# Kernel optimization log

Hardware: AMD Instinct MI355X
Metric: run time of the kernel (lower is better)

Reference implementation:

```python
import jax, jax.numpy as jnp
import numpy as np

DIM = 256
HEADS = 8
HEAD_DIM = DIM // HEADS
WS = 7            # window size
SHIFT = 3         # shift size
H = 56
W = 56
B = 32
WA = WS * WS      # window area = 49
NWH, NWW = H // WS, W // WS
NW = NWH * NWW    # windows per image


def _make_attn_mask():
    # replicate the torch mask construction for the shifted windows
    img = np.zeros((H, W), dtype=np.float32)
    cnt = 0
    for hs in (slice(0, -WS), slice(-WS, -SHIFT), slice(-SHIFT, None)):
        for ws_ in (slice(0, -WS), slice(-WS, -SHIFT), slice(-SHIFT, None)):
            img[hs, ws_] = cnt
            cnt += 1
    mw = img.reshape(NWH, WS, NWW, WS).transpose(0, 2, 1, 3).reshape(-1, WA)  # (nW, 49)
    diff = mw[:, None, :] - mw[:, :, None]                                    # (nW, 49, 49)
    return np.where(diff != 0, -100.0, 0.0).astype(np.float32)


def _make_rel_index():
    coords = np.stack(np.meshgrid(np.arange(WS), np.arange(WS), indexing='ij')).reshape(2, -1)
    rel = coords[:, :, None] - coords[:, None, :]        # (2, 49, 49)
    rel = rel.transpose(1, 2, 0) + (WS - 1)              # shift to >= 0
    rel[..., 0] *= 2 * WS - 1
    return rel.sum(-1).astype(np.int32)                  # (49, 49) in [0, 169)


def setup_inputs() -> dict:
    key = jax.random.key(0)
    ks = jax.random.split(key, 12)
    s = 0.02
    inp = {
        'x': jax.random.normal(ks[0], (B, H, W, DIM), dtype=jnp.float32),
        'ln1_w': jnp.ones((DIM,), jnp.float32), 'ln1_b': jnp.zeros((DIM,), jnp.float32),
        'qkv_w': s * jax.random.normal(ks[1], (3 * DIM, DIM), jnp.float32),
        'qkv_b': jnp.zeros((3 * DIM,), jnp.float32),
        'rpb_table': s * jax.random.normal(ks[2], ((2 * WS - 1) ** 2, HEADS), jnp.float32),
        'proj_w': s * jax.random.normal(ks[3], (DIM, DIM), jnp.float32),
        'proj_b': jnp.zeros((DIM,), jnp.float32),
        'ln2_w': jnp.ones((DIM,), jnp.float32), 'ln2_b': jnp.zeros((DIM,), jnp.float32),
        'fc1_w': s * jax.random.normal(ks[4], (4 * DIM, DIM), jnp.float32),
        'fc1_b': jnp.zeros((4 * DIM,), jnp.float32),
        'ln3_w': jnp.ones((4 * DIM,), jnp.float32), 'ln3_b': jnp.zeros((4 * DIM,), jnp.float32),
        'fc2_w': s * jax.random.normal(ks[5], (DIM, 4 * DIM), jnp.float32),
        'fc2_b': jnp.zeros((DIM,), jnp.float32),
        'attn_mask': jnp.asarray(_make_attn_mask()),     # (nW, 49, 49)
        'rel_index': jnp.asarray(_make_rel_index()),     # (49, 49) int32
    }
    return inp


def _ln(x, w, b, eps=1e-5):
    m = jnp.mean(x, axis=-1, keepdims=True)
    v = jnp.mean((x - m) ** 2, axis=-1, keepdims=True)
    return (x - m) * jax.lax.rsqrt(v + eps) * w + b


def reference(x, ln1_w, ln1_b, qkv_w, qkv_b, rpb_table, proj_w, proj_b,
              ln2_w, ln2_b, fc1_w, fc1_b, ln3_w, ln3_b, fc2_w, fc2_b,
              attn_mask, rel_index):
    Bn, Hn, Wn, C = x.shape
    # ---- attention branch ----
    y = _ln(x, ln1_w, ln1_b)
    sh = jnp.roll(y, (-SHIFT, -SHIFT), axis=(1, 2))
    # window partition: (B, H, W, C) -> (B*nW, 49, C)
    win = sh.reshape(Bn, NWH, WS, NWW, WS, C).transpose(0, 1, 3, 2, 4, 5).reshape(Bn * NW, WA, C)
    qkv = win @ qkv_w.T + qkv_b                              # (Bw, 49, 3C)
    qkv = qkv.reshape(Bn * NW, WA, 3, HEADS, HEAD_DIM).transpose(2, 0, 3, 1, 4)
    q, k, v = qkv[0], qkv[1], qkv[2]                         # (Bw, h, 49, d)
    scale = HEAD_DIM ** -0.5
    attn = jnp.einsum('bhqd,bhkd->bhqk', q * scale, k)       # (Bw, h, 49, 49)
    bias = rpb_table[rel_index]                              # (49, 49, h)
    attn = attn + jnp.transpose(bias, (2, 0, 1))[None]
    attn = attn.reshape(Bn, NW, HEADS, WA, WA) + attn_mask[None, :, None]
    attn = jax.nn.softmax(attn, axis=-1).reshape(Bn * NW, HEADS, WA, WA)
    out = jnp.einsum('bhqk,bhkd->bhqd', attn, v)             # (Bw, h, 49, d)
    out = out.transpose(0, 2, 1, 3).reshape(Bn * NW, WA, C)
    out = out @ proj_w.T + proj_b
    # window reverse + un-shift
    out = out.reshape(Bn, NWH, NWW, WS, WS, C).transpose(0, 1, 3, 2, 4, 5).reshape(Bn, Hn, Wn, C)
    out = jnp.roll(out, (SHIFT, SHIFT), axis=(1, 2))
    x = x + out
    # ---- MLP branch (note: extra LayerNorm inside MLP per source) ----
    z = _ln(x, ln2_w, ln2_b)
    h = jax.nn.gelu(z @ fc1_w.T + fc1_b, approximate=False)
    h = _ln(h, ln3_w, ln3_b)
    x = x + (h @ fc2_w.T + fc2_b)
    return x
```

## Files before the change

### kernel.cpp

```cpp
#include <hip/hip_runtime.h>
#include <hip/hip_bf16.h>
#include <math.h>

typedef __attribute__((ext_vector_type(8))) short bf16x8;
typedef __attribute__((ext_vector_type(4))) float f32x4;
typedef __attribute__((ext_vector_type(4))) float f4;
typedef __attribute__((ext_vector_type(8))) unsigned short us8;
typedef __attribute__((ext_vector_type(4))) unsigned short us4;
typedef unsigned short u16;
typedef unsigned int u32;

#define HEADS 8
#define SHIFT_ 3
#define HIMG 56
#define WIMG 56
#define WA 49
#define NTOK 100352
#define NPAIR 16384

static __device__ __forceinline__ float bf2f(u16 v){ return __uint_as_float(((u32)v)<<16); }
static __device__ __forceinline__ u16 f2bf(float f){
  u32 u = __float_as_uint(f);
  return (u16)((u + 0x7fffu + ((u>>16)&1u)) >> 16);
}
static __device__ __forceinline__ float wsum(float v){
  #pragma unroll
  for (int off=32; off>0; off>>=1) v += __shfl_xor(v, off, 64);
  return v;
}
static __device__ __forceinline__ void glds16(const u16* g, u16* l){
  __builtin_amdgcn_global_load_lds(
      (const __attribute__((address_space(1))) unsigned int*)g,
      (__attribute__((address_space(3))) unsigned int*)l, 16, 0, 0);
}
static __device__ __forceinline__ int tok2pix(int row){
  int bw = row / 49, t = row - bw*49;
  int b  = bw >> 6,  w = bw & 63;
  int wh = w >> 3,   ww = w & 7;
  int th = t / 7,    tw = t - th*7;
  int r = wh*7 + th + SHIFT_; if (r >= HIMG) r -= HIMG;
  int c = ww*7 + tw + SHIFT_; if (c >= WIMG) c -= WIMG;
  return (b*HIMG + r)*WIMG + c;
}

template<int C, int ISBF>
__global__ void ln_stats_kernel(const void* __restrict__ srcv, float* __restrict__ stats){
  int wave = threadIdx.x >> 6, lane = threadIdx.x & 63;
  int tok = blockIdx.x*4 + wave;
  float s=0.f, s2=0.f;
  if (ISBF == 0){
    const float* p = (const float*)srcv + (size_t)tok*C;
    #pragma unroll
    for (int i=0;i<C/256;i++){
      f4 v = *(const f4*)(p + lane*4*(C/256) + i*4);
      #pragma unroll
      for (int e=0;e<4;e++){ float f=v[e]; s+=f; s2+=f*f; }
    }
  } else {
    const u16* p = (const u16*)srcv + (size_t)tok*C;
    #pragma unroll
    for (int i=0;i<C/512;i++){
      us8 v = *(const us8*)(p + lane*8*(C/512) + i*8);
      #pragma unroll
      for (int e=0;e<8;e++){ float f=bf2f(v[e]); s+=f; s2+=f*f; }
    }
  }
  s = wsum(s); s2 = wsum(s2);
  if (lane==0){
    float mean = s/(float)C;
    float var  = s2/(float)C - mean*mean;
    stats[2*tok]   = mean;
    stats[2*tok+1] = rsqrtf(var + 1e-5f);
  }
}

__global__ void ln_apply_kernel(const float* __restrict__ src, u16* __restrict__ dst){
  int wave = threadIdx.x >> 6, lane = threadIdx.x & 63;
  int tok = blockIdx.x*4 + wave;
  const float* p = src + (size_t)tok*256;
  f4 a = *(const f4*)(p + lane*4);
  float s = a[0]+a[1]+a[2]+a[3];
  float s2 = a[0]*a[0]+a[1]*a[1]+a[2]*a[2]+a[3]*a[3];
  s = wsum(s); s2 = wsum(s2);
  float mean = s*(1.f/256.f);
  float var  = s2*(1.f/256.f) - mean*mean;
  float rstd = rsqrtf(var + 1e-5f);
  us4 o;
  #pragma unroll
  for (int e=0;e<4;e++) o[e] = f2bf((a[e]-mean)*rstd);
  *(us4*)(dst + (size_t)tok*256 + lane*4) = o;
}

__global__ void prep_weights(
    const float* __restrict__ qkv_w, const float* __restrict__ qkv_b,
    const float* __restrict__ ln1w,  const float* __restrict__ ln1b,
    const float* __restrict__ fc1_w, const float* __restrict__ fc1_b,
    const float* __restrict__ ln2w,  const float* __restrict__ ln2b,
    const float* __restrict__ fc2_w, const float* __restrict__ fc2_b,
    const float* __restrict__ ln3w,  const float* __restrict__ ln3b,
    const float* __restrict__ proj_w, const float* __restrict__ proj_b,
    u16* __restrict__ wq, float* __restrict__ bq,
    u16* __restrict__ w1, float* __restrict__ b1,
    u16* __restrict__ w2, float* __restrict__ b2,
    u16* __restrict__ wp, float* __restrict__ bp)
{
  int wave = threadIdx.x>>6, lane = threadIdx.x&63;
  int n = blockIdx.x*4 + wave;
  const float *W,*lw,*lb,*bs; u16* WO; float* BO; int K, row, noln;
  if (n < 768)      { W=qkv_w; lw=ln1w; lb=ln1b; bs=qkv_b; WO=wq; BO=bq; K=256;  row=n;      noln=0; }
  else if (n < 1792){ W=fc1_w; lw=ln2w; lb=ln2b; bs=fc1_b; WO=w1; BO=b1; K=256;  row=n-768;  noln=0; }
  else if (n < 2048){ W=fc2_w; lw=ln3w; lb=ln3b; bs=fc2_b; WO=w2; BO=b2; K=1024; row=n-1792; noln=0; }
  else              { W=proj_w; lw=nullptr; lb=nullptr; bs=proj_b; WO=wp; BO=bp; K=256; row=n-2048; noln=1; }
  float dot = 0.f;
  for (int k=lane; k<K; k+=64){
    float wv = W[(size_t)row*K + k];
    if (noln){
      WO[(size_t)row*K + k] = f2bf(wv);
    } else {
      dot += wv * lb[k];
      WO[(size_t)row*K + k] = f2bf(wv * lw[k]);
    }
  }
  dot = wsum(dot);
  if (lane==0) BO[row] = bs[row] + dot;
}

template<int SMODE, int EPI>
__global__ __launch_bounds__(256)
void gemm4(const void* __restrict__ Av, const u16* __restrict__ Bt,
           const float* __restrict__ stats, const float* __restrict__ biasf,
           const float* __restrict__ resid, void* __restrict__ outv,
           int K, int NT, int CHUNK)
{
  constexpr int BM=128, BN=128, BK=64;
  __shared__ u16 smem[32768];
  int b = blockIdx.x;
  int linear = (b & 7)*CHUNK + (b >> 3);
  int mt = linear / NT, nt = linear - mt*NT;
  int m0 = mt*BM, n0 = nt*BN;
  int tid  = threadIdx.x;
  int lane = tid & 63, wave = tid >> 6;
  int wr = wave >> 1, wc = wave & 1;
  int lc16 = lane & 15, g = lane >> 4;
  int nsteps = K >> 6;

  const u16* asrc[4];
  const u16* bsrc[4];
  #pragma unroll
  for (int i=0;i<4;i++){
    int c = tid + i*256;
    int row = c >> 3, ch = (c & 7) ^ (row & 7);
    if (SMODE <= 1){
      int grow = (SMODE==0) ? tok2pix(m0+row) : (m0+row);
      asrc[i] = (const u16*)Av + (size_t)grow*K + ch*8;
    }
    bsrc[i] = Bt + (size_t)(n0+row)*K + ch*8;
  }
  float smean[4], srstd[4];
  if (SMODE >= 2){
    #pragma unroll
    for (int i=0;i<4;i++){
      int grow = m0 + ((tid + i*256) >> 3);
      smean[i] = stats[2*grow]; srstd[i] = stats[2*grow+1];
    }
  }

  f32x4 acc[4][4];
  #pragma unroll
  for (int i=0;i<4;i++)
    #pragma unroll
    for (int j=0;j<4;j++){ acc[i][j][0]=0.f; acc[i][j][1]=0.f; acc[i][j][2]=0.f; acc[i][j][3]=0.f; }

  us8 rcur[4]; f4 rcurf[4][2];
  if (SMODE <= 1){
    #pragma unroll
    for (int i=0;i<4;i++) glds16(asrc[i], smem + i*2048 + wave*512);
  } else {
    #pragma unroll
    for (int i=0;i<4;i++){
      int c = tid + i*256; int row = c>>3, ch = c&7;
      if (SMODE==2) rcur[i] = *(const us8*)((const u16*)Av + (size_t)(m0+row)*K + ch*8);
      else {
        const float* ap = (const float*)Av + (size_t)(m0+row)*K + ch*8;
        rcurf[i][0] = *(const f4*)ap; rcurf[i][1] = *(const f4*)(ap+4);
      }
    }
  }
  #pragma unroll
  for (int i=0;i<4;i++) glds16(bsrc[i], smem + 16384 + i*2048 + wave*512);

  for (int t=0; t<nsteps; ++t){
    int cur = t & 1;
    int curoff = cur << 13;
    int nxtoff = (cur^1) << 13;
    us8 rnext[4]; f4 rnextf[4][2];
    int kt1 = (t+1) << 6;
    if (t+1 < nsteps){
      if (SMODE <= 1){
        #pragma unroll
        for (int i=0;i<4;i++) glds16(asrc[i]+kt1, smem + nxtoff + i*2048 + wave*512);
      } else {
        #pragma unroll
        for (int i=0;i<4;i++){
          int c = tid + i*256; int row = c>>3, ch = c&7;
          if (SMODE==2) rnext[i] = *(const us8*)((const u16*)Av + (size_t)(m0+row)*K + kt1 + ch*8);
          else {
            const float* ap = (const float*)Av + (size_t)(m0+row)*K + kt1 + ch*8;
            rnextf[i][0] = *(const f4*)ap; rnextf[i][1] = *(const f4*)(ap+4);
          }
        }
      }
      #pragma unroll
      for (int i=0;i<4;i++) glds16(bsrc[i]+kt1, smem + 16384 + nxtoff + i*2048 + wave*512);
    }
    if (SMODE >= 2){
      #pragma unroll
      for (int i=0;i<4;i++){
        int c = tid + i*256; int row = c>>3, ch = c&7;
        us8 o;
        #pragma unroll
        for (int e=0;e<8;e++){
          float fv = (SMODE==2) ? bf2f(rcur[i][e]) : rcurf[i][e>>2][e&3];
          o[e] = f2bf((fv - smean[i])*srstd[i]);
        }
        u32 byte = (u32)(row*128 + ch*16) ^ ((u32)(row&7)<<4);
        *(us8*)(smem + curoff + (byte>>1)) = o;
      }
      asm volatile("s_waitcnt lgkmcnt(0)" ::: "memory");
    }
    if (t+1 < nsteps) asm volatile("s_waitcnt vmcnt(8)" ::: "memory");
    else              asm volatile("s_waitcnt vmcnt(0)" ::: "memory");
    __builtin_amdgcn_s_barrier();
    asm volatile("" ::: "memory");
    __builtin_amdgcn_sched_barrier(0);
    const u16* Ap = smem + curoff;
    const u16* Bp = smem + 16384 + curoff;
    #pragma unroll
    for (int kk=0; kk<2; kk++){
      bf16x8 af[4], bfr[4];
      #pragma unroll
      for (int mi=0;mi<4;mi++){
        int r = wr*64 + mi*16 + lc16;
        u32 byte = (u32)(r*128 + kk*64 + g*16) ^ ((u32)(r&7)<<4);
        af[mi] = *(const bf16x8*)(Ap + (byte>>1));
      }
      #pragma unroll
      for (int ni=0;ni<4;ni++){
        int r = wc*64 + ni*16 + lc16;
        u32 byte = (u32)(r*128 + kk*64 + g*16) ^ ((u32)(r&7)<<4);
        bfr[ni] = *(const bf16x8*)(Bp + (byte>>1));
      }
      #pragma unroll
      for (int mi=0;mi<4;mi++)
        #pragma unroll
        for (int ni=0;ni<4;ni++)
          acc[mi][ni] = __builtin_amdgcn_mfma_f32_16x16x32_bf16(af[mi], bfr[ni], acc[mi][ni], 0, 0, 0);
    }
    asm volatile("" ::: "memory");
    __builtin_amdgcn_s_barrier();
    asm volatile("" ::: "memory");
    if (SMODE >= 2 && t+1 < nsteps){
      #pragma unroll
      for (int i=0;i<4;i++){
        if (SMODE==2) rcur[i] = rnext[i];
        else { rcurf[i][0] = rnextf[i][0]; rcurf[i][1] = rnextf[i][1]; }
      }
    }
  }

  int lr = lane >> 4;
  if (EPI==0 || EPI==2){
    u16* Cs = smem;
    #pragma unroll
    for (int mi=0;mi<4;mi++){
      #pragma unroll
      for (int ni=0;ni<4;ni++){
        int cl = wc*64 + ni*16 + lc16;
        float bv = biasf[n0 + cl];
        #pragma unroll
        for (int j=0;j<4;j++){
          int rl = wr*64 + mi*16 + lr*4 + j;
          float v = acc[mi][ni][j] + bv;
          if (EPI==2) v = 0.5f*v*(1.f + erff(v*0.70710678118654752f));
          u32 byte = (u32)(rl*256 + cl*2) ^ ((u32)(rl&7)<<4);
          Cs[byte>>1] = f2bf(v);
        }
      }
    }
    __syncthreads();
    #pragma unroll
    for (int i=0;i<8;i++){
      int c = tid + i*256;
      int rl = c>>4, c0 = (c&15)*8;
      u32 byte = (u32)(rl*256 + c0*2) ^ ((u32)(rl&7)<<4);
      us8 v = *(const us8*)(Cs + (byte>>1));
      int row = m0 + rl, col = n0 + c0;
      if (EPI==0){
        int which = col>>8, hh = (col>>5)&7, d0 = col&31;
        int bwi = row/49, t = row - bwi*49;
        *(us8*)((u16*)outv + ((size_t)which*NPAIR + bwi*8 + hh)*(WA*32) + t*32 + d0) = v;
      } else {
        *(us8*)((u16*)outv + (size_t)row*1024 + col) = v;
      }
    }
  } else {
    float* Cs = (float*)smem;
    #pragma unroll
    for (int mi=0;mi<4;mi++){
      #pragma unroll
      for (int ni=0;ni<4;ni++){
        int cl = wc*64 + ni*16 + lc16;
        float bv = biasf[n0 + cl];
        #pragma unroll
        for (int j=0;j<4;j++){
          int rl = wr*64 + mi*16 + lr*4 + j;
          u32 byte = (u32)(rl*512 + cl*4) ^ ((u32)(rl&7)<<4);
          *(float*)((char*)Cs + byte) = acc[mi][ni][j] + bv;
        }
      }
    }
    __syncthreads();
    #pragma unroll
    for (int p=0;p<16;p++){
      int c = tid + p*256;
      int row = c>>5, ch = c&31;
      u32 byte = (u32)(row*512 + ch*16) ^ ((u32)(row&7)<<4);
      f4 v = *(const f4*)((const char*)Cs + byte);
      int grow = m0 + row, col = n0 + ch*4;
      size_t addr;
      if (EPI==1) addr = (size_t)tok2pix(grow)*256 + col;
      else        addr = (size_t)grow*256 + col;
      f4 rr = *(const f4*)(resid + addr);
      v += rr;
      *(f4*)((float*)outv + addr) = v;
    }
  }
}

__global__ void attn_mfma_kernel(
    const u16* __restrict__ qkv,
    const float* __restrict__ rpb,
    const int* __restrict__ rel,
    const float* __restrict__ mask,
    u16* __restrict__ outb)
{
  __shared__ u16 Kls[4][64*32];
  __shared__ u16 Vt [4][32*64];
  __shared__ u16 Pls[4][64*64];
  int wave = threadIdx.x>>6, lane = threadIdx.x&63;
  int pair = blockIdx.x*4 + wave;
  int bw = pair>>3, h = pair&7, w = bw&63;
  int lc = lane&15, g = lane>>4;
  const u16* qg = qkv + (size_t)pair*(WA*32);
  const u16* kg = qg + (size_t)NPAIR*(WA*32);
  const u16* vg = qg + (size_t)2*NPAIR*(WA*32);
  u16* Kp = &Kls[wave][0];
  u16* Vp = &Vt[wave][0];
  u16* Pp = &Pls[wave][0];

  #pragma unroll
  for (int i=0;i<4;i++){
    int idx = i*64 + lane;
    int r = idx>>2, seg = idx&3;
    us8 kv, vv;
    if (r < WA){
      kv = *(const us8*)(kg + r*32 + seg*8);
      vv = *(const us8*)(vg + r*32 + seg*8);
    } else {
      #pragma unroll
      for (int e=0;e<8;e++){ kv[e]=0; vv[e]=0; }
    }
    *(us8*)(Kp + r*32 + seg*8) = kv;
    #pragma unroll
    for (int e=0;e<8;e++){
      int d = seg*8 + e;
      u32 byte = ((u32)(d*128 + r*2)) ^ ((u32)(d&7)<<4);
      Vp[byte>>1] = vv[e];
    }
  }

  bf16x8 qa[4];
  #pragma unroll
  for (int mi=0;mi<4;mi++){
    int r = mi*16 + lc;
    if (r < WA) qa[mi] = *(const bf16x8*)(qg + r*32 + g*8);
    else { bf16x8 z;
           #pragma unroll
           for (int e=0;e<8;e++) z[e]=0; qa[mi]=z; }
  }

  f32x4 acc[4][4];
  #pragma unroll
  for (int i=0;i<4;i++)
    #pragma unroll
    for (int j=0;j<4;j++){ acc[i][j][0]=0.f; acc[i][j][1]=0.f; acc[i][j][2]=0.f; acc[i][j][3]=0.f; }
  __syncthreads();
  #pragma unroll
  for (int ni=0;ni<4;ni++){
    bf16x8 kb = *(const bf16x8*)(Kp + (ni*16+lc)*32 + g*8);
    #pragma unroll
    for (int mi=0;mi<4;mi++)
      acc[mi][ni] = __builtin_amdgcn_mfma_f32_16x16x32_bf16(qa[mi], kb, acc[mi][ni], 0, 0, 0);
  }

  const float scale = 0.17677669529663689f;
  float rinv[4][4];
  #pragma unroll
  for (int mi=0;mi<4;mi++){
    #pragma unroll
    for (int jr=0;jr<4;jr++){
      int i = mi*16 + g*4 + jr;
      float sv[4];
      #pragma unroll
      for (int ni=0;ni<4;ni++){
        int j = ni*16 + lc;
        float s;
        if (i < WA && j < WA){
          s = acc[mi][ni][jr]*scale + rpb[rel[i*WA+j]*8 + h] + mask[((size_t)w*WA + i)*WA + j];
        } else s = -1e9f;
        sv[ni] = s;
      }
      float mx = fmaxf(fmaxf(sv[0],sv[1]), fmaxf(sv[2],sv[3]));
      #pragma unroll
      for (int off=1; off<16; off<<=1) mx = fmaxf(mx, __shfl_xor(mx, off, 64));
      float sum = 0.f;
      #pragma unroll
      for (int ni=0;ni<4;ni++){ sv[ni] = __expf(sv[ni]-mx); sum += sv[ni]; }
      #pragma unroll
      for (int off=1; off<16; off<<=1) sum += __shfl_xor(sum, off, 64);
      rinv[mi][jr] = 1.f/sum;
      #pragma unroll
      for (int ni=0;ni<4;ni++){
        int j = ni*16 + lc;
        u32 byte = ((u32)(i*128 + j*2)) ^ ((u32)(i&7)<<4);
        Pp[byte>>1] = f2bf(sv[ni]);
      }
    }
  }

  bf16x8 vb[2][2];
  #pragma unroll
  for (int kk=0;kk<2;kk++)
    #pragma unroll
    for (int ni=0;ni<2;ni++){
      int d = ni*16 + lc;
      u32 byte = ((u32)(d*128 + kk*64 + g*16)) ^ ((u32)(d&7)<<4);
      vb[kk][ni] = *(const bf16x8*)(Vp + (byte>>1));
    }
  f32x4 aco[4][2];
  #pragma unroll
  for (int i=0;i<4;i++)
    #pragma unroll
    for (int j=0;j<2;j++){ aco[i][j][0]=0.f; aco[i][j][1]=0.f; aco[i][j][2]=0.f; aco[i][j][3]=0.f; }
  #pragma unroll
  for (int mi=0;mi<4;mi++){
    int r = mi*16 + lc;
    #pragma unroll
    for (int kk=0;kk<2;kk++){
      u32 byte = ((u32)(r*128 + kk*64 + g*16)) ^ ((u32)(r&7)<<4);
      bf16x8 pa = *(const bf16x8*)(Pp + (byte>>1));
      #pragma unroll
      for (int ni=0;ni<2;ni++)
        aco[mi][ni] = __builtin_amdgcn_mfma_f32_16x16x32_bf16(pa, vb[kk][ni], aco[mi][ni], 0, 0, 0);
    }
  }

  u16* Op = Kp;
  #pragma unroll
  for (int mi=0;mi<4;mi++){
    #pragma unroll
    for (int jr=0;jr<4;jr++){
      int i = mi*16 + g*4 + jr;
      if (i < WA){
        float rv = rinv[mi][jr];
        #pragma unroll
        for (int ni=0;ni<2;ni++)
          Op[i*32 + ni*16 + lc] = f2bf(aco[mi][ni][jr]*rv);
      }
    }
  }
  __syncthreads();
  size_t obase = (size_t)(bw*WA)*256 + h*32;
  #pragma unroll
  for (int i=0;i<4;i++){
    int c = i*64 + lane;
    if (c < WA*4){
      int t = c>>2, seg = c&3;
      *(us8*)(outb + obase + (size_t)t*256 + seg*8) = *(const us8*)(Op + t*32 + seg*8);
    }
  }
}

extern "C" void kernel_launch(void* const* d_in, const int* in_sizes, int n_in,
                              void* d_out, int out_size, void* d_ws, size_t ws_size,
                              hipStream_t stream) {
  const float* x      = (const float*)d_in[0];
  const float* ln1w   = (const float*)d_in[1];
  const float* ln1b   = (const float*)d_in[2];
  const float* qkv_w  = (const float*)d_in[3];
  const float* qkv_b  = (const float*)d_in[4];
  const float* rpb    = (const float*)d_in[5];
  const float* proj_w = (const float*)d_in[6];
  const float* proj_b = (const float*)d_in[7];
  const float* ln2w   = (const float*)d_in[8];
  const float* ln2b   = (const float*)d_in[9];
  const float* fc1_w  = (const float*)d_in[10];
  const float* fc1_b  = (const float*)d_in[11];
  const float* ln3w   = (const float*)d_in[12];
  const float* ln3b   = (const float*)d_in[13];
  const float* fc2_w  = (const float*)d_in[14];
  const float* fc2_b  = (const float*)d_in[15];
  const float* amask  = (const float*)d_in[16];
  const int*   rel    = (const int*)d_in[17];
  float* out = (float*)d_out;

  char* ws = (char*)d_ws;
  float* statsC = (float*)(ws);
  float* statsB = (float*)(ws +  802816);
  float* bq     = (float*)(ws + 1605632);
  float* b1     = (float*)(ws + 1608704);
  float* b2     = (float*)(ws + 1612800);
  float* bp     = (float*)(ws + 1613824);
  u16*   wq     = (u16*)  (ws + 1614848);
  u16*   w1     = (u16*)  (ws + 2008064);
  u16*   w2     = (u16*)  (ws + 2532352);
  u16*   wp     = (u16*)  (ws + 3056640);
  const size_t P0 = 3187712;
  u16*   qkvbuf = (u16*)(ws + P0);
  u16*   attno  = (u16*)(ws + P0 + 154140672);
  u16*   xb     = (u16*)(ws + P0 + 154140672);
  u16*   hbuf   = (u16*)(ws + P0);
  u16*   x1b    = (u16*)(ws + P0 + 205520896);
  const int bigws = (ws_size >= (size_t)(P0 + 205520896ull + 51380224ull));

  prep_weights<<<576,256,0,stream>>>(qkv_w,qkv_b,ln1w,ln1b, fc1_w,fc1_b,ln2w,ln2b,
                                     fc2_w,fc2_b,ln3w,ln3b, proj_w,proj_b,
                                     wq,bq, w1,b1, w2,b2, wp,bp);
  ln_apply_kernel<<<NTOK/4,256,0,stream>>>(x, xb);
  gemm4<0,0><<<784*6,256,0,stream>>>(xb, wq, nullptr, bq, nullptr, qkvbuf, 256, 6, 588);
  attn_mfma_kernel<<<NPAIR/4,256,0,stream>>>(qkvbuf, rpb, rel, amask, attno);
  gemm4<1,1><<<784*2,256,0,stream>>>(attno, wp, nullptr, bp, x, out, 256, 2, 196);
  if (bigws){
    ln_apply_kernel<<<NTOK/4,256,0,stream>>>(out, x1b);
    gemm4<1,2><<<784*8,256,0,stream>>>(x1b, w1, nullptr, b1, nullptr, hbuf, 256, 8, 784);
  } else {
    ln_stats_kernel<256,0><<<NTOK/4,256,0,stream>>>(out, statsB);
    gemm4<3,2><<<784*8,256,0,stream>>>(out, w1, statsB, b1, nullptr, hbuf, 256, 8, 784);
  }
  ln_stats_kernel<1024,1><<<NTOK/4,256,0,stream>>>(hbuf, statsC);
  gemm4<2,3><<<784*2,256,0,stream>>>(hbuf, w2, statsC, b2, out, out, 1024, 2, 196);
}
```

Baseline: 625.8 us.

## Single-buffer GEMM LDS to raise occupancy, use polynomial GELU and fast reciprocal

Halves the GEMM shared memory by dropping LDS double buffering, switching to a load-sync-compute loop, and requests four blocks per CU through launch bounds. The fp32 epilogue is split into two 64-column halves so it fits the smaller LDS buffer. Exact erf GELU is replaced with an Abramowitz-Stegun polynomial approximation, and the softmax division uses the hardware reciprocal. The goal is more resident waves to hide latency, at the cost of losing the explicit prefetch overlap inside each block and a slight loss of accuracy.

```diff
diff --git a/kernel.cpp b/kernel.cpp
--- a/kernel.cpp
+++ b/kernel.cpp
@@ -41,6 +41,15 @@
   int r = wh*7 + th + SHIFT_; if (r >= HIMG) r -= HIMG;
   int c = ww*7 + tw + SHIFT_; if (c >= WIMG) c -= WIMG;
   return (b*HIMG + r)*WIMG + c;
+}
+static __device__ __forceinline__ float gelu_f(float x){
+  float z  = 0.70710678118654752f * x;
+  float az = fabsf(z);
+  float t  = __builtin_amdgcn_rcpf(1.0f + 0.3275911f*az);
+  float p  = t*(0.254829592f + t*(-0.284496736f + t*(1.421413741f + t*(-1.453152027f + t*1.061405429f))));
+  float er = 1.0f - p*__expf(-z*z);
+  er = (x < 0.0f) ? -er : er;
+  return 0.5f*x*(1.0f + er);
 }
 
 template<int C, int ISBF>
@@ -126,14 +135,16 @@
 }
 
 template<int SMODE, int EPI>
-__global__ __launch_bounds__(256)
-void gemm4(const void* __restrict__ Av, const u16* __restrict__ Bt,
+__global__ __launch_bounds__(256,4)
+void gemm5(const void* __restrict__ Av, const u16* __restrict__ Bt,
            const float* __restrict__ stats, const float* __restrict__ biasf,
            const float* __restrict__ resid, void* __restrict__ outv,
            int K, int NT, int CHUNK)
 {
   constexpr int BM=128, BN=128, BK=64;
-  __shared__ u16 smem[32768];
+  __shared__ u16 smem[16384];
+  u16* As = smem;
+  u16* Bs = smem + 8192;
   int b = blockIdx.x;
   int linear = (b & 7)*CHUNK + (b >> 3);
   int mt = linear / NT, nt = linear - mt*NT;
@@ -172,10 +183,7 @@
     for (int j=0;j<4;j++){ acc[i][j][0]=0.f; acc[i][j][1]=0.f; acc[i][j][2]=0.f; acc[i][j][3]=0.f; }
 
   us8 rcur[4]; f4 rcurf[4][2];
-  if (SMODE <= 1){
-    #pragma unroll
-    for (int i=0;i<4;i++) glds16(asrc[i], smem + i*2048 + wave*512);
-  } else {
+  if (SMODE >= 2){
     #pragma unroll
     for (int i=0;i<4;i++){
       int c = tid + i*256; int row = c>>3, ch = c&7;
@@ -186,34 +194,13 @@
       }
     }
   }
-  #pragma unroll
-  for (int i=0;i<4;i++) glds16(bsrc[i], smem + 16384 + i*2048 + wave*512);
 
   for (int t=0; t<nsteps; ++t){
-    int cur = t & 1;
-    int curoff = cur << 13;
-    int nxtoff = (cur^1) << 13;
-    us8 rnext[4]; f4 rnextf[4][2];
-    int kt1 = (t+1) << 6;
-    if (t+1 < nsteps){
-      if (SMODE <= 1){
-        #pragma unroll
-        for (int i=0;i<4;i++) glds16(asrc[i]+kt1, smem + nxtoff + i*2048 + wave*512);
-      } else {
-        #pragma unroll
-        for (int i=0;i<4;i++){
-          int c = tid + i*256; int row = c>>3, ch = c&7;
-          if (SMODE==2) rnext[i] = *(const us8*)((const u16*)Av + (size_t)(m0+row)*K + kt1 + ch*8);
-          else {
-            const float* ap = (const float*)Av + (size_t)(m0+row)*K + kt1 + ch*8;
-            rnextf[i][0] = *(const f4*)ap; rnextf[i][1] = *(const f4*)(ap+4);
-          }
-        }
-      }
-      #pragma unroll
-      for (int i=0;i<4;i++) glds16(bsrc[i]+kt1, smem + 16384 + nxtoff + i*2048 + wave*512);
-    }
-    if (SMODE >= 2){
+    int kt = t << 6;
+    if (SMODE <= 1){
+      #pragma unroll
+      for (int i=0;i<4;i++) glds16(asrc[i]+kt, As + i*2048 + wave*512);
+    } else {
       #pragma unroll
       for (int i=0;i<4;i++){
         int c = tid + i*256; int row = c>>3, ch = c&7;
@@ -224,48 +211,74 @@
           o[e] = f2bf((fv - smean[i])*srstd[i]);
         }
         u32 byte = (u32)(row*128 + ch*16) ^ ((u32)(row&7)<<4);
-        *(us8*)(smem + curoff + (byte>>1)) = o;
-      }
-      asm volatile("s_waitcnt lgkmcnt(0)" ::: "memory");
-    }
-    if (t+1 < nsteps) asm volatile("s_waitcnt vmcnt(8)" ::: "memory");
-    else              asm volatile("s_waitcnt vmcnt(0)" ::: "memory");
-    __builtin_amdgcn_s_barrier();
-    asm volatile("" ::: "memory");
-    __builtin_amdgcn_sched_barrier(0);
-    const u16* Ap = smem + curoff;
-    const u16* Bp = smem + 16384 + curoff;
-    #pragma unroll
-    for (int kk=0; kk<2; kk++){
-      bf16x8 af[4], bfr[4];
-      #pragma unroll
-      for (int mi=0;mi<4;mi++){
-        int r = wr*64 + mi*16 + lc16;
-        u32 byte = (u32)(r*128 + kk*64 + g*16) ^ ((u32)(r&7)<<4);
-        af[mi] = *(const bf16x8*)(Ap + (byte>>1));
-      }
-      #pragma unroll
-      for (int ni=0;ni<4;ni++){
-        int r = wc*64 + ni*16 + lc16;
-        u32 byte = (u32)(r*128 + kk*64 + g*16) ^ ((u32)(r&7)<<4);
-        bfr[ni] = *(const bf16x8*)(Bp + (byte>>1));
-      }
-      #pragma unroll
-      for (int mi=0;mi<4;mi++)
-        #pragma unroll
-        for (int ni=0;ni<4;ni++)
-          acc[mi][ni] = __builtin_amdgcn_mfma_f32_16x16x32_bf16(af[mi], bfr[ni], acc[mi][ni], 0, 0, 0);
-    }
-    asm volatile("" ::: "memory");
-    __builtin_amdgcn_s_barrier();
-    asm volatile("" ::: "memory");
+        *(us8*)(As + (byte>>1)) = o;
+      }
+    }
+    #pragma unroll
+    for (int i=0;i<4;i++) glds16(bsrc[i]+kt, Bs + i*2048 + wave*512);
+    __syncthreads();
     if (SMODE >= 2 && t+1 < nsteps){
+      int kt1 = kt + 64;
+      us8 rnext[4]; f4 rnextf[4][2];
+      #pragma unroll
+      for (int i=0;i<4;i++){
+        int c = tid + i*256; int row = c>>3, ch = c&7;
+        if (SMODE==2) rnext[i] = *(const us8*)((const u16*)Av + (size_t)(m0+row)*K + kt1 + ch*8);
+        else {
+          const float* ap = (const float*)Av + (size_t)(m0+row)*K + kt1 + ch*8;
+          rnextf[i][0] = *(const f4*)ap; rnextf[i][1] = *(const f4*)(ap+4);
+        }
+      }
+      #pragma unroll
+      for (int kk=0; kk<2; kk++){
+        bf16x8 af[4], bfr[4];
+        #pragma unroll
+        for (int mi=0;mi<4;mi++){
+          int r = wr*64 + mi*16 + lc16;
+          u32 byte = (u32)(r*128 + kk*64 + g*16) ^ ((u32)(r&7)<<4);
+          af[mi] = *(const bf16x8*)(As + (byte>>1));
+        }
+        #pragma unroll
+        for (int ni=0;ni<4;ni++){
+          int r = wc*64 + ni*16 + lc16;
+          u32 byte = (u32)(r*128 + kk*64 + g*16) ^ ((u32)(r&7)<<4);
+          bfr[ni] = *(const bf16x8*)(Bs + (byte>>1));
+        }
+        #pragma unroll
+        for (int mi=0;mi<4;mi++)
+          #pragma unroll
+          for (int ni=0;ni<4;ni++)
+            acc[mi][ni] = __builtin_amdgcn_mfma_f32_16x16x32_bf16(af[mi], bfr[ni], acc[mi][ni], 0, 0, 0);
+      }
       #pragma unroll
       for (int i=0;i<4;i++){
         if (SMODE==2) rcur[i] = rnext[i];
         else { rcurf[i][0] = rnextf[i][0]; rcurf[i][1] = rnextf[i][1]; }
       }
-    }
+    } else {
+      #pragma unroll
+      for (int kk=0; kk<2; kk++){
+        bf16x8 af[4], bfr[4];
+        #pragma unroll
+        for (int mi=0;mi<4;mi++){
+          int r = wr*64 + mi*16 + lc16;
+          u32 byte = (u32)(r*128 + kk*64 + g*16) ^ ((u32)(r&7)<<4);
+          af[mi] = *(const bf16x8*)(As + (byte>>1));
+        }
+        #pragma unroll
+        for (int ni=0;ni<4;ni++){
+          int r = wc*64 + ni*16 + lc16;
+          u32 byte = (u32)(r*128 + kk*64 + g*16) ^ ((u32)(r&7)<<4);
+          bfr[ni] = *(const bf16x8*)(Bs + (byte>>1));
+        }
+        #pragma unroll
+        for (int mi=0;mi<4;mi++)
+          #pragma unroll
+          for (int ni=0;ni<4;ni++)
+            acc[mi][ni] = __builtin_amdgcn_mfma_f32_16x16x32_bf16(af[mi], bfr[ni], acc[mi][ni], 0, 0, 0);
+      }
+    }
+    __syncthreads();
   }
 
   int lr = lane >> 4;
@@ -281,7 +294,7 @@
         for (int j=0;j<4;j++){
           int rl = wr*64 + mi*16 + lr*4 + j;
           float v = acc[mi][ni][j] + bv;
-          if (EPI==2) v = 0.5f*v*(1.f + erff(v*0.70710678118654752f));
+          if (EPI==2) v = gelu_f(v);
           u32 byte = (u32)(rl*256 + cl*2) ^ ((u32)(rl&7)<<4);
           Cs[byte>>1] = f2bf(v);
         }
@@ -306,33 +319,39 @@
   } else {
     float* Cs = (float*)smem;
     #pragma unroll
-    for (int mi=0;mi<4;mi++){
-      #pragma unroll
-      for (int ni=0;ni<4;ni++){
-        int cl = wc*64 + ni*16 + lc16;
-        float bv = biasf[n0 + cl];
-        #pragma unroll
-        for (int j=0;j<4;j++){
-          int rl = wr*64 + mi*16 + lr*4 + j;
-          u32 byte = (u32)(rl*512 + cl*4) ^ ((u32)(rl&7)<<4);
-          *(float*)((char*)Cs + byte) = acc[mi][ni][j] + bv;
-        }
-      }
-    }
-    __syncthreads();
-    #pragma unroll
-    for (int p=0;p<16;p++){
-      int c = tid + p*256;
-      int row = c>>5, ch = c&31;
-      u32 byte = (u32)(row*512 + ch*16) ^ ((u32)(row&7)<<4);
-      f4 v = *(const f4*)((const char*)Cs + byte);
-      int grow = m0 + row, col = n0 + ch*4;
-      size_t addr;
-      if (EPI==1) addr = (size_t)tok2pix(grow)*256 + col;
-      else        addr = (size_t)grow*256 + col;
-      f4 rr = *(const f4*)(resid + addr);
-      v += rr;
-      *(f4*)((float*)outv + addr) = v;
+    for (int hp=0; hp<2; hp++){
+      if (hp) __syncthreads();
+      if (wc == hp){
+        #pragma unroll
+        for (int mi=0;mi<4;mi++){
+          #pragma unroll
+          for (int ni=0;ni<4;ni++){
+            int cl = ni*16 + lc16;
+            float bv = biasf[n0 + hp*64 + cl];
+            #pragma unroll
+            for (int j=0;j<4;j++){
+              int rl = wr*64 + mi*16 + lr*4 + j;
+              u32 byte = (u32)(rl*256 + cl*4) ^ ((u32)(rl&7)<<4);
+              *(float*)((char*)Cs + byte) = acc[mi][ni][j] + bv;
+            }
+          }
+        }
+      }
+      __syncthreads();
+      #pragma unroll
+      for (int i=0;i<8;i++){
+        int c = tid + i*256;
+        int row = c>>4, ch = c&15;
+        u32 byte = (u32)(row*256 + ch*16) ^ ((u32)(row&7)<<4);
+        f4 v = *(const f4*)((const char*)Cs + byte);
+        int grow = m0 + row, col = n0 + hp*64 + ch*4;
+        size_t addr;
+        if (EPI==1) addr = (size_t)tok2pix(grow)*256 + col;
+        else        addr = (size_t)grow*256 + col;
+        f4 rr = *(const f4*)(resid + addr);
+        v += rr;
+        *(f4*)((float*)outv + addr) = v;
+      }
     }
   }
 }
@@ -428,7 +447,7 @@
       for (int ni=0;ni<4;ni++){ sv[ni] = __expf(sv[ni]-mx); sum += sv[ni]; }
       #pragma unroll
       for (int off=1; off<16; off<<=1) sum += __shfl_xor(sum, off, 64);
-      rinv[mi][jr] = 1.f/sum;
+      rinv[mi][jr] = __builtin_amdgcn_rcpf(sum);
       #pragma unroll
       for (int ni=0;ni<4;ni++){
         int j = ni*16 + lc;
@@ -537,16 +556,16 @@
                                      fc2_w,fc2_b,ln3w,ln3b, proj_w,proj_b,
                                      wq,bq, w1,b1, w2,b2, wp,bp);
   ln_apply_kernel<<<NTOK/4,256,0,stream>>>(x, xb);
-  gemm4<0,0><<<784*6,256,0,stream>>>(xb, wq, nullptr, bq, nullptr, qkvbuf, 256, 6, 588);
+  gemm5<0,0><<<784*6,256,0,stream>>>(xb, wq, nullptr, bq, nullptr, qkvbuf, 256, 6, 588);
   attn_mfma_kernel<<<NPAIR/4,256,0,stream>>>(qkvbuf, rpb, rel, amask, attno);
-  gemm4<1,1><<<784*2,256,0,stream>>>(attno, wp, nullptr, bp, x, out, 256, 2, 196);
+  gemm5<1,1><<<784*2,256,0,stream>>>(attno, wp, nullptr, bp, x, out, 256, 2, 196);
   if (bigws){
     ln_apply_kernel<<<NTOK/4,256,0,stream>>>(out, x1b);
-    gemm4<1,2><<<784*8,256,0,stream>>>(x1b, w1, nullptr, b1, nullptr, hbuf, 256, 8, 784);
+    gemm5<1,2><<<784*8,256,0,stream>>>(x1b, w1, nullptr, b1, nullptr, hbuf, 256, 8, 784);
   } else {
     ln_stats_kernel<256,0><<<NTOK/4,256,0,stream>>>(out, statsB);
-    gemm4<3,2><<<784*8,256,0,stream>>>(out, w1, statsB, b1, nullptr, hbuf, 256, 8, 784);
+    gemm5<3,2><<<784*8,256,0,stream>>>(out, w1, statsB, b1, nullptr, hbuf, 256, 8, 784);
   }
   ln_stats_kernel<1024,1><<<NTOK/4,256,0,stream>>>(hbuf, statsC);
-  gemm4<2,3><<<784*2,256,0,stream>>>(hbuf, w2, statsC, b2, out, out, 1024, 2, 196);
-}
+  gemm5<2,3><<<784*2,256,0,stream>>>(hbuf, w2, statsC, b2, out, out, 1024, 2, 196);
+}
```

After: 1.263 ms. 102% more time.
